# Performance work log

Hardware: AMD Instinct MI355X
Metric: run time of the kernel (lower is better)

The kernel has to match this reference:

```python
import jax, jax.numpy as jnp
import numpy as np

NUM_CLASSES = 8192
FEAT_DIM = 256
BATCH = 4096


def setup_inputs() -> dict:
    key = jax.random.key(0)
    kx, kl, kc = jax.random.split(key, 3)
    x = jax.random.normal(kx, (BATCH, FEAT_DIM), dtype=jnp.float32)
    labels = jax.random.randint(kl, (BATCH,), 0, NUM_CLASSES, dtype=jnp.int64)
    centers = jax.random.normal(kc, (NUM_CLASSES, FEAT_DIM), dtype=jnp.float32)
    return {"x": x, "labels": labels, "centers": centers}


def reference(x, labels, centers):
    # distmat[b, c] = ||x_b||^2 + ||center_c||^2 - 2 x_b . center_c  -> [B, C]
    distmat = (
        jnp.sum(x * x, axis=1, keepdims=True)
        + jnp.sum(centers * centers, axis=1)[None, :]
        - 2.0 * jnp.einsum("bd,cd->bc", x, centers)
    )
    # mask selects each sample's own class column
    mask = (labels[:, None] == jnp.arange(centers.shape[0])[None, :]).astype(distmat.dtype)
    dist = distmat * mask
    # Faithful to reference: clamp is applied AFTER masking, so zeroed entries
    # become 1e-12 and contribute B*(C-1)*1e-12 to the sum.
    loss = jnp.clip(dist, 1e-12, 1e12).sum() / x.shape[0]
    return loss
```

## Files before the change

kernel.cpp:

```cpp
#include <hip/hip_runtime.h>

#define BATCH 4096
#define FEAT_DIM 256
#define NUM_CLASSES 8192

#define WAVES_PER_BLOCK 16
#define SAMPLES_PER_WAVE 4
#define THREADS (WAVES_PER_BLOCK * 64)
#define NBLOCKS (BATCH / (WAVES_PER_BLOCK * SAMPLES_PER_WAVE))

__global__ __launch_bounds__(THREADS) void CenterLoss_77378130805013_kernel(
    const float* __restrict__ x,
    const int* __restrict__ labels,
    const float* __restrict__ centers,
    float* __restrict__ out)
{
    const int wave = threadIdx.x >> 6;
    const int lane = threadIdx.x & 63;
    const int wave_id = blockIdx.x * WAVES_PER_BLOCK + wave;
    const int b0 = wave_id * SAMPLES_PER_WAVE;

    const int4 l4 = *(const int4*)(labels + b0);
    const int lbl[SAMPLES_PER_WAVE] = {l4.x, l4.y, l4.z, l4.w};

    float4 xv[SAMPLES_PER_WAVE], cv[SAMPLES_PER_WAVE];
    #pragma unroll
    for (int i = 0; i < SAMPLES_PER_WAVE; ++i)
        xv[i] = ((const float4*)(x + (size_t)(b0 + i) * FEAT_DIM))[lane];
    #pragma unroll
    for (int i = 0; i < SAMPLES_PER_WAVE; ++i)
        cv[i] = ((const float4*)(centers + (size_t)lbl[i] * FEAT_DIM))[lane];

    float acc = 0.0f;
    #pragma unroll
    for (int i = 0; i < SAMPLES_PER_WAVE; ++i) {
        const float d0 = xv[i].x - cv[i].x;
        const float d1 = xv[i].y - cv[i].y;
        const float d2 = xv[i].z - cv[i].z;
        const float d3 = xv[i].w - cv[i].w;
        acc += d0 * d0 + d1 * d1 + d2 * d2 + d3 * d3;
    }

    #pragma unroll
    for (int off = 32; off > 0; off >>= 1)
        acc += __shfl_down(acc, off, 64);

    __shared__ float wsum[WAVES_PER_BLOCK];
    if (lane == 0) wsum[wave] = acc;
    __syncthreads();

    if (wave == 0) {
        float v = (lane < WAVES_PER_BLOCK) ? wsum[lane] : 0.0f;
        #pragma unroll
        for (int off = 8; off > 0; off >>= 1)
            v += __shfl_down(v, off, 64);
        if (lane == 0) {
            v *= (1.0f / (float)BATCH);
            if (blockIdx.x == 0)
                v += (float)((NUM_CLASSES - 1) * 1e-12);
            atomicAdd(out, v);
        }
    }
}

extern "C" void kernel_launch(void* const* d_in, const int* in_sizes, int n_in,
                              void* d_out, int out_size, void* d_ws, size_t ws_size,
                              hipStream_t stream) {
    const float* x       = (const float*)d_in[0];
    const int*   labels  = (const int*)d_in[1];
    const float* centers = (const float*)d_in[2];
    float* out = (float*)d_out;

    CenterLoss_77378130805013_kernel<<<dim3(NBLOCKS), dim3(THREADS), 0, stream>>>(
        x, labels, centers, out);
}
```

Before: 63.70 us.

## Replace global atomic accumulation with two-pass partial-sum reduction kernel

Splits the reduction into two kernels. The first writes one partial sum per block to workspace using smaller 256-thread blocks (256 blocks instead of 64). A second single-wave kernel sums the partials and writes the final value directly. This removes the atomicAdd into an output that presumably had to be zeroed beforehand, and gives more blocks to spread across CUs. In exchange it adds a second kernel launch and its dependency latency.

```diff
diff --git a/kernel.cpp b/kernel.cpp
--- a/kernel.cpp
+++ b/kernel.cpp
@@ -4,36 +4,35 @@
 #define FEAT_DIM 256
 #define NUM_CLASSES 8192
 
-#define WAVES_PER_BLOCK 16
-#define SAMPLES_PER_WAVE 4
-#define THREADS (WAVES_PER_BLOCK * 64)
-#define NBLOCKS (BATCH / (WAVES_PER_BLOCK * SAMPLES_PER_WAVE))
+#define K1_BLOCKS 256
+#define K1_WAVES 4
+#define K1_SAMPLES 4
+#define K1_THREADS (K1_WAVES * 64)
 
-__global__ __launch_bounds__(THREADS) void CenterLoss_77378130805013_kernel(
+__global__ __launch_bounds__(K1_THREADS) void CenterLoss_77378130805013_partial(
     const float* __restrict__ x,
     const int* __restrict__ labels,
     const float* __restrict__ centers,
-    float* __restrict__ out)
+    float* __restrict__ ws)
 {
     const int wave = threadIdx.x >> 6;
     const int lane = threadIdx.x & 63;
-    const int wave_id = blockIdx.x * WAVES_PER_BLOCK + wave;
-    const int b0 = wave_id * SAMPLES_PER_WAVE;
+    const int b0 = (blockIdx.x * K1_WAVES + wave) * K1_SAMPLES;
 
     const int4 l4 = *(const int4*)(labels + b0);
-    const int lbl[SAMPLES_PER_WAVE] = {l4.x, l4.y, l4.z, l4.w};
+    const int lbl[K1_SAMPLES] = {l4.x, l4.y, l4.z, l4.w};
 
-    float4 xv[SAMPLES_PER_WAVE], cv[SAMPLES_PER_WAVE];
+    float4 xv[K1_SAMPLES], cv[K1_SAMPLES];
     #pragma unroll
-    for (int i = 0; i < SAMPLES_PER_WAVE; ++i)
+    for (int i = 0; i < K1_SAMPLES; ++i)
         xv[i] = ((const float4*)(x + (size_t)(b0 + i) * FEAT_DIM))[lane];
     #pragma unroll
-    for (int i = 0; i < SAMPLES_PER_WAVE; ++i)
+    for (int i = 0; i < K1_SAMPLES; ++i)
         cv[i] = ((const float4*)(centers + (size_t)lbl[i] * FEAT_DIM))[lane];
 
     float acc = 0.0f;
     #pragma unroll
-    for (int i = 0; i < SAMPLES_PER_WAVE; ++i) {
+    for (int i = 0; i < K1_SAMPLES; ++i) {
         const float d0 = xv[i].x - cv[i].x;
         const float d1 = xv[i].y - cv[i].y;
         const float d2 = xv[i].z - cv[i].z;
@@ -45,22 +44,27 @@
     for (int off = 32; off > 0; off >>= 1)
         acc += __shfl_down(acc, off, 64);
 
-    __shared__ float wsum[WAVES_PER_BLOCK];
+    __shared__ float wsum[K1_WAVES];
     if (lane == 0) wsum[wave] = acc;
     __syncthreads();
 
-    if (wave == 0) {
-        float v = (lane < WAVES_PER_BLOCK) ? wsum[lane] : 0.0f;
-        #pragma unroll
-        for (int off = 8; off > 0; off >>= 1)
-            v += __shfl_down(v, off, 64);
-        if (lane == 0) {
-            v *= (1.0f / (float)BATCH);
-            if (blockIdx.x == 0)
-                v += (float)((NUM_CLASSES - 1) * 1e-12);
-            atomicAdd(out, v);
-        }
-    }
+    if (threadIdx.x == 0)
+        ws[blockIdx.x] = wsum[0] + wsum[1] + wsum[2] + wsum[3];
+}
+
+__global__ __launch_bounds__(64) void CenterLoss_77378130805013_final(
+    const float* __restrict__ ws,
+    float* __restrict__ out)
+{
+    const int lane = threadIdx.x;
+    const float4 v = ((const float4*)ws)[lane];
+    float s = v.x + v.y + v.z + v.w;
+    #pragma unroll
+    for (int off = 32; off > 0; off >>= 1)
+        s += __shfl_down(s, off, 64);
+    if (lane == 0)
+        out[0] = s * (1.0f / (float)BATCH)
+               + (float)((NUM_CLASSES - 1) * 1e-12);
 }
 
 extern "C" void kernel_launch(void* const* d_in, const int* in_sizes, int n_in,
@@ -69,8 +73,10 @@
     const float* x       = (const float*)d_in[0];
     const int*   labels  = (const int*)d_in[1];
     const float* centers = (const float*)d_in[2];
+    float* ws  = (float*)d_ws;
     float* out = (float*)d_out;
 
-    CenterLoss_77378130805013_kernel<<<dim3(NBLOCKS), dim3(THREADS), 0, stream>>>(
-        x, labels, centers, out);
+    CenterLoss_77378130805013_partial<<<dim3(K1_BLOCKS), dim3(K1_THREADS), 0, stream>>>(
+        x, labels, centers, ws);
+    CenterLoss_77378130805013_final<<<dim3(1), dim3(64), 0, stream>>>(ws, out);
 }
```

Result: no change. 64.53 us (+1.3%).
